# Performance work log

Measured on AMD Instinct MI355X. Metric: run time of the kernel, lower is better.

Reference implementation:

```python
import jax, jax.numpy as jnp
import numpy as np
from jax import lax

EPS = 1e-6


def _layernorm(x, g, b, eps=1e-5):
    m = x.mean(-1, keepdims=True)
    v = x.var(-1, keepdims=True)
    return (x - m) / jnp.sqrt(v + eps) * g + b


def _causal_conv(x, w, b, dilation):
    # x: [B,S,D], w: [K, D_in, D_out] -> causal (left) padded dilated conv + GELU, residual
    k = w.shape[0]
    pad = (k - 1) * dilation
    y = lax.conv_general_dilated(
        x, w, window_strides=(1,), padding=[(pad, 0)], rhs_dilation=(dilation,),
        dimension_numbers=('NWC', 'WIO', 'NWC'))
    return x + jax.nn.gelu(y + b)


def setup_inputs() -> dict:
    key = jax.random.key(0)
    B, S, D, DC, N_LTM, K_WM, KS = 4, 2048, 1024, 256, 768, 8, 5
    ks = jax.random.split(key, 24)
    sc = 0.02

    def n(k, shape, scale=sc):
        return jax.random.normal(k, shape, jnp.float32) * scale

    return {
        'x': jax.random.normal(ks[0], (B, S, D), jnp.float32),
        'cache': jax.random.normal(ks[1], (B, N_LTM, DC), jnp.float32),
        'wm': jax.random.normal(ks[2], (B, K_WM, DC + 1), jnp.float32),
        # LTM read projections
        'Wq_ltm': n(ks[3], (D, DC)), 'Wo_ltm': n(ks[4], (DC, D)), 'wg_ltm': n(ks[5], (D,)),
        # WM read projections
        'Wq_wm': n(ks[6], (D, DC)), 'Wo_wm': n(ks[7], (DC, D)), 'wg_wm': n(ks[8], (D,)),
        # causal dilated conv stack (2 layers, k=5, dilations 1 and 2)
        'conv1_w': n(ks[9], (KS, D, D)), 'conv1_b': jnp.zeros((D,), jnp.float32),
        'conv2_w': n(ks[10], (KS, D, D)), 'conv2_b': jnp.zeros((D,), jnp.float32),
        'ln_g': jnp.ones((D,), jnp.float32), 'ln_b': jnp.zeros((D,), jnp.float32),
        # WM write (learned slot keys for addressing)
        'Wqw_wm': n(ks[11], (D, DC)), 'Ww_wm': n(ks[12], (D, DC)),
        'wm_keys': n(ks[13], (K_WM, DC), 1.0), 'wgw_wm': n(ks[14], (D,)),
        # LTM write (content-based addressing against cache)
        'Wqw_ltm': n(ks[15], (D, DC)), 'Ww_ltm': n(ks[16], (D, DC)), 'wgw_ltm': n(ks[17], (D,)),
    }


def reference(x, cache, wm, Wq_ltm, Wo_ltm, wg_ltm, Wq_wm, Wo_wm, wg_wm,
              conv1_w, conv1_b, conv2_w, conv2_b, ln_g, ln_b,
              Wqw_wm, Ww_wm, wm_keys, wgw_wm, Wqw_ltm, Ww_ltm, wgw_ltm):
    DC = cache.shape[-1]
    inv_sqrt = 1.0 / jnp.sqrt(jnp.float32(DC))

    # ---- LTM READ: content-addressed soft read, gated residual blend ----
    q = x @ Wq_ltm                                                  # [B,S,DC]
    attn = jax.nn.softmax(jnp.einsum('bsd,bnd->bsn', q, cache) * inv_sqrt, -1)
    read = jnp.einsum('bsn,bnd->bsd', attn, cache)                  # [B,S,DC]
    gate = jax.nn.sigmoid(x @ wg_ltm)[..., None]                    # [B,S,1]
    x_ltm = x + gate * (read @ Wo_ltm)

    # ---- WM READ (read_decay=0.0 -> wm unchanged by read) ----
    content = wm[..., :DC]                                          # [B,Kw,DC]
    q2 = x_ltm @ Wq_wm
    attn2 = jax.nn.softmax(jnp.einsum('bsd,bkd->bsk', q2, content) * inv_sqrt, -1)
    read2 = jnp.einsum('bsk,bkd->bsd', attn2, content)
    gate2 = jax.nn.sigmoid(x_ltm @ wg_wm)[..., None]
    x_enh = x_ltm + gate2 * (read2 @ Wo_wm)

    # ---- COMPUTE: causal dilated conv stack + post-LayerNorm ----
    h = _causal_conv(x_enh, conv1_w, conv1_b, 1)
    h = _causal_conv(h, conv2_w, conv2_b, 2)
    out = _layernorm(h, ln_g, ln_b)                                 # [B,S,D]

    # ---- WM WRITE: gated soft-WTA addressing vs learned slot keys ----
    qw = out @ Wqw_wm                                               # [B,S,DC]
    aw = jax.nn.softmax(jnp.einsum('bsd,kd->bsk', qw, wm_keys) * inv_sqrt, -1)
    gw = jax.nn.sigmoid(out @ wgw_wm)[..., None]                    # [B,S,1]
    w = gw * aw                                                     # [B,S,Kw]
    tot = w.sum(1)                                                  # [B,Kw]
    c = out @ Ww_wm                                                 # [B,S,DC]
    avg = jnp.einsum('bsk,bsd->bkd', w, c) / (tot[..., None] + EPS)
    alpha = jnp.clip(tot, 0.0, 1.0)[..., None]
    new_content = (1.0 - alpha) * content + alpha * avg
    new_valid = jnp.clip(wm[..., DC] + tot, 0.0, 1.0)               # validity channel
    updated_wm = jnp.concatenate([new_content, new_valid[..., None]], -1)

    # ---- LTM WRITE: gated soft blended write, content-addressed vs cache ----
    ql = out @ Wqw_ltm
    al = jax.nn.softmax(jnp.einsum('bsd,bnd->bsn', ql, cache) * inv_sqrt, -1)
    gl = jax.nn.sigmoid(out @ wgw_ltm)[..., None]
    wl = gl * al                                                    # [B,S,N]
    totl = wl.sum(1)                                                # [B,N]
    cl = out @ Ww_ltm
    avgl = jnp.einsum('bsn,bsd->bnd', wl, cl) / (totl[..., None] + EPS)
    alphal = jnp.clip(totl, 0.0, 1.0)[..., None]
    updated_cache = (1.0 - alphal) * cache + alphal * avgl

    return (out, updated_cache, updated_wm)
```

## Files before the change

kernel.cpp:

```cpp
#include <hip/hip_runtime.h>
#include <stdint.h>

typedef unsigned short u16;
typedef unsigned int u32;
typedef __attribute__((ext_vector_type(8))) short s16x8;
typedef __attribute__((ext_vector_type(4))) float f32x4;

__device__ __forceinline__ float bf2f(u16 u) {
    return __builtin_bit_cast(float, (u32)u << 16);
}
__device__ __forceinline__ u16 f2bf(float f) {
    u32 u = __builtin_bit_cast(u32, f);
    u += 0x7FFFu + ((u >> 16) & 1u);
    return (u16)(u >> 16);
}
__device__ __forceinline__ void unpk4(uint2 r, float* o) {
    o[0] = bf2f((u16)(r.x & 0xffff)); o[1] = bf2f((u16)(r.x >> 16));
    o[2] = bf2f((u16)(r.y & 0xffff)); o[3] = bf2f((u16)(r.y >> 16));
}

__device__ __forceinline__ void gl16(const u16* g, u16* l) {
    __builtin_amdgcn_global_load_lds(
        (const __attribute__((address_space(1))) u32*)(const void*)g,
        (__attribute__((address_space(3))) u32*)(void*)l, 16, 0, 0);
}

#define BAR() { __builtin_amdgcn_sched_barrier(0); __builtin_amdgcn_s_barrier(); __builtin_amdgcn_sched_barrier(0); }

template<int DIL>
__global__ __launch_bounds__(512) void conv8_k(
    const u16* __restrict__ Apad, const u16* __restrict__ Bw,
    u16* __restrict__ Cb0, u16* __restrict__ Cb1)
{
    __shared__ u16 sA[2][16384];
    __shared__ u16 sB[2][16384];
    const int tid  = threadIdx.x;
    const int wid  = tid >> 6;
    const int lane = tid & 63;
    const int wr = (wid >> 2) * 128;
    const int wc = (wid & 3) * 64;
    const int lr = lane & 15;
    const int kq = lane >> 4;
    const int batch = blockIdx.x >> 3;
    const int m0b   = (blockIdx.x & 7) * 256;
    const int bn0   = blockIdx.y * 256;
    const int kbeg  = blockIdx.z * 2560;
    const u16* Ab = Apad + (long)batch * 2056 * 1024;

    const int row0 = tid >> 3;
    const int g0   = (tid & 7) ^ (row0 & 7);

    f32x4 acc[8][4] = {};
    s16x8 aF[4][2], bF[4][2];

    auto stageA = [&](int nb, int kt, int h) {
        const int ktabs = kbeg + kt * 64;
        const int tap = ktabs >> 10;
        const long rbase = (long)(8 + m0b + h * 128 + (tap - 4) * DIL) * 1024
                           + (ktabs & 1023) + g0 * 8;
        u16* dst = &sA[nb][h * 8192 + tid * 8];
        gl16(Ab + rbase + (long)row0 * 1024, dst);
        gl16(Ab + rbase + (long)(row0 + 64) * 1024, dst + 4096);
    };
    auto stageB = [&](int nb, int kt, int h) {
        const int ktabs = kbeg + kt * 64;
        const long rbase = (long)(bn0 + h * 128) * 5120 + ktabs + g0 * 8;
        u16* dst = &sB[nb][h * 8192 + tid * 8];
        gl16(Bw + rbase + (long)row0 * 5120, dst);
        gl16(Bw + rbase + (long)(row0 + 64) * 5120, dst + 4096);
    };
    auto readA = [&](int nb, int mq) {
        #pragma unroll
        for (int m = 0; m < 4; m++) {
            const int row = wr + (mq * 4 + m) * 16 + lr;
            #pragma unroll
            for (int ks = 0; ks < 2; ks++) {
                const int chunk = ks * 4 + kq;
                aF[m][ks] = *(const s16x8*)&sA[nb][row * 64 + ((chunk ^ (row & 7)) << 3)];
            }
        }
    };
    auto readB4 = [&](int nb, int nq) {
        #pragma unroll
        for (int n = 0; n < 2; n++) {
            const int row = wc + (nq * 2 + n) * 16 + lr;
            #pragma unroll
            for (int ks = 0; ks < 2; ks++) {
                const int chunk = ks * 4 + kq;
                bF[nq * 2 + n][ks] = *(const s16x8*)&sB[nb][row * 64 + ((chunk ^ (row & 7)) << 3)];
            }
        }
    };

#define MFQ(MQ, NQ) \
    { __builtin_amdgcn_s_setprio(1); \
      _Pragma("unroll") \
      for (int m = 0; m < 4; m++) { \
        _Pragma("unroll") \
        for (int n = 0; n < 2; n++) { \
          _Pragma("unroll") \
          for (int ks = 0; ks < 2; ks++) \
            acc[(MQ)*4+m][(NQ)*2+n] = __builtin_amdgcn_mfma_f32_16x16x32_bf16( \
                aF[m][ks], bF[(NQ)*2+n][ks], acc[(MQ)*4+m][(NQ)*2+n], 0, 0, 0); \
        } } \
      __builtin_amdgcn_s_setprio(0); }

    stageB(0, 0, 0); stageB(0, 0, 1); stageA(0, 0, 0); stageA(0, 0, 1);

    const int NT = 40;
    for (int t = 0; t < NT; ++t) {
        const int nb = t & 1;
        asm volatile("s_waitcnt vmcnt(4)" ::: "memory");
        BAR();
        readB4(nb, 0); readB4(nb, 1);
        if (t + 1 < NT) { stageB(nb ^ 1, t + 1, 0); stageB(nb ^ 1, t + 1, 1); }
        if (t + 1 < NT) { asm volatile("s_waitcnt vmcnt(4)" ::: "memory"); }
        else            { asm volatile("s_waitcnt vmcnt(0)" ::: "memory"); }
        BAR();
        readA(nb, 0);
        MFQ(0, 0); MFQ(0, 1);
        if (t + 1 < NT) { stageA(nb ^ 1, t + 1, 0); stageA(nb ^ 1, t + 1, 1); }
        readA(nb, 1);
        MFQ(1, 0); MFQ(1, 1);
    }
#undef MFQ

    u16* C = (blockIdx.z ? Cb1 : Cb0) + (long)batch * 2048 * 1024;
    #pragma unroll
    for (int m = 0; m < 8; m++) {
        #pragma unroll
        for (int n = 0; n < 4; n++) {
            const int cc = bn0 + wc + n * 16 + lr;
            #pragma unroll
            for (int j = 0; j < 4; j++) {
                const int r = m0b + wr + m * 16 + kq * 4 + j;
                C[(long)r * 1024 + cc] = f2bf(acc[m][n][j]);
            }
        }
    }
}

template<int AL, int BL, int EPI, int TN, int KS, int SWZ>
__global__ __launch_bounds__(256) void gemm_bf16(
    const u16* __restrict__ A, const u16* __restrict__ B,
    float* __restrict__ Cf, u16* __restrict__ Cb,
    const float* __restrict__ res, const float* __restrict__ gate,
    int M, int N, int K, int lda, int ldb,
    long aBS, long bBS, long cBS,
    u16* __restrict__ Pp, long pStride, int nby)
{
    constexpr int NFRAG = TN / 32;
    __shared__ u16 sA[128 * 32];
    __shared__ u16 sB[TN * 32];
    const int tid  = threadIdx.x;
    const int lane = tid & 63;
    const int wave = tid >> 6;
    const int wr = (wave >> 1) * 64;
    const int wc = (wave & 1) * (TN / 2);

    int bidx, bidy;
    if (SWZ) {
        const int nb  = gridDim.x;
        const int cpx = nb >> 3;
        const int bf  = blockIdx.x;
        const int sw  = (bf & 7) * cpx + (bf >> 3);
        bidx = sw / nby; bidy = sw - bidx * nby;
    } else {
        bidx = blockIdx.x; bidy = blockIdx.y;
    }
    const int m0 = bidx * 128;
    const int n0 = bidy * TN;
    const int zz = blockIdx.z;
    const long bz = (KS > 1) ? (zz / KS) : zz;
    const int ks  = (KS > 1) ? (zz % KS) : 0;
    const u16* Ab = A + bz * aBS;
    const u16* Bb = B + bz * bBS;

    f32x4 acc[4][NFRAG] = {};
    const int lr = lane & 15;
    const int lk = (lane >> 4) << 3;
    const int ar0 = tid >> 2;
    const int akg = (tid & 3) << 3;

    const int Kp = K / KS;
    const int kbeg = ks * Kp, kend = kbeg + Kp;

    for (int kk = kbeg; kk < kend; kk += 32) {
        __syncthreads();
        if (AL == 0) {
            gl16(Ab + (long)(m0 + ar0) * lda + kk + akg,      sA + tid * 8);
            gl16(Ab + (long)(m0 + ar0 + 64) * lda + kk + akg, sA + tid * 8 + 2048);
        } else {
            for (int t = tid; t < 512; t += 256) {
                int row = t & 127, kg = (t >> 7) << 3;
                u32 w0[4];
                #pragma unroll
                for (int j2 = 0; j2 < 4; j2++) {
                    u16 lo = Ab[(long)(kk + kg + 2*j2    ) * lda + m0 + row];
                    u16 hi = Ab[(long)(kk + kg + 2*j2 + 1) * lda + m0 + row];
                    w0[j2] = (u32)lo | ((u32)hi << 16);
                }
                uint4 v; v.x = w0[0]; v.y = w0[1]; v.z = w0[2]; v.w = w0[3];
                *reinterpret_cast<uint4*>(sA + row * 32 + kg) = v;
            }
        }
        if (BL == 1) {
            gl16(Bb + (long)(n0 + ar0) * ldb + kk + akg, sB + tid * 8);
            if (TN == 128)
                gl16(Bb + (long)(n0 + ar0 + 64) * ldb + kk + akg, sB + tid * 8 + 2048);
        } else {
            for (int t = tid; t < TN * 4; t += 256) {
                int col = t & (TN - 1), kg = (t / TN) << 3;
                u32 w0[4];
                #pragma unroll
                for (int j2 = 0; j2 < 4; j2++) {
                    u16 lo = Bb[(long)(kk + kg + 2*j2    ) * ldb + n0 + col];
                    u16 hi = Bb[(long)(kk + kg + 2*j2 + 1) * ldb + n0 + col];
                    w0[j2] = (u32)lo | ((u32)hi << 16);
                }
                uint4 v; v.x = w0[0]; v.y = w0[1]; v.z = w0[2]; v.w = w0[3];
                *reinterpret_cast<uint4*>(sB + col * 32 + kg) = v;
            }
        }
        __syncthreads();
        s16x8 aF[4], bF[NFRAG];
        #pragma unroll
        for (int m = 0; m < 4; m++)
            aF[m] = *reinterpret_cast<const s16x8*>(sA + (wr + m*16 + lr) * 32 + lk);
        #pragma unroll
        for (int n = 0; n < NFRAG; n++)
            bF[n] = *reinterpret_cast<const s16x8*>(sB + (wc + n*16 + lr) * 32 + lk);
        #pragma unroll
        for (int m = 0; m < 4; m++)
            #pragma unroll
            for (int n = 0; n < NFRAG; n++)
                acc[m][n] = __builtin_amdgcn_mfma_f32_16x16x32_bf16(aF[m], bF[n], acc[m][n], 0, 0, 0);
    }

    const int rj = (lane >> 4) << 2;
    if (KS > 1) {
        u16* Pb = Pp + (long)ks * pStride + bz * cBS;
        #pragma unroll
        for (int m = 0; m < 4; m++)
            #pragma unroll
            for (int n = 0; n < NFRAG; n++) {
                const int cc = n0 + wc + n*16 + lr;
                #pragma unroll
                for (int j = 0; j < 4; j++) {
                    const int r = m0 + wr + m*16 + rj + j;
                    Pb[(long)r * N + cc] = f2bf(acc[m][n][j]);
                }
            }
        return;
    }

    float* Cfb = Cf + bz * cBS;
    #pragma unroll
    for (int m = 0; m < 4; m++) {
        #pragma unroll
        for (int n = 0; n < NFRAG; n++) {
            const int cc = n0 + wc + n*16 + lr;
            #pragma unroll
            for (int j = 0; j < 4; j++) {
                const int r = m0 + wr + m*16 + rj + j;
                const long idx = (long)r * N + cc;
                const float v = acc[m][n][j];
                if (EPI == 0) {
                    Cb[bz * cBS + idx] = f2bf(v);
                } else if (EPI == 1) {
                    Cfb[idx] = v;
                } else {
                    float o = res[idx] + gate[r] * v;
                    Cfb[idx] = o;
                    if (EPI == 2) Cb[idx] = f2bf(o);
                }
            }
        }
    }
}

template<int KS, int BF>
__global__ __launch_bounds__(256) void ksum_k(
    const u16* __restrict__ Pp, long pStride,
    float* __restrict__ outf, u16* __restrict__ outb, int n4)
{
    int i = blockIdx.x * 256 + threadIdx.x;
    if (i >= n4) return;
    float s[4] = {0.f, 0.f, 0.f, 0.f};
    #pragma unroll
    for (int k = 0; k < KS; k++) {
        uint2 r = reinterpret_cast<const uint2*>(Pp + (long)k * pStride)[i];
        float v[4]; unpk4(r, v);
        s[0] += v[0]; s[1] += v[1]; s[2] += v[2]; s[3] += v[3];
    }
    if (BF) {
        u32 lo = (u32)f2bf(s[0]) | ((u32)f2bf(s[1]) << 16);
        u32 hi = (u32)f2bf(s[2]) | ((u32)f2bf(s[3]) << 16);
        reinterpret_cast<uint2*>(outb)[i] = make_uint2(lo, hi);
    } else {
        float4 o; o.x = s[0]; o.y = s[1]; o.z = s[2]; o.w = s[3];
        reinterpret_cast<float4*>(outf)[i] = o;
    }
}

__global__ __launch_bounds__(256) void prep_k(
    const float* __restrict__ x, const float* __restrict__ cache,
    const float* __restrict__ wm_keys, const float* __restrict__ wm,
    const float* __restrict__ Wo_wm, const float* __restrict__ Wq_wm,
    const float* __restrict__ Wq_ltm, const float* __restrict__ Wqw_wm,
    const float* __restrict__ Ww_wm, const float* __restrict__ Wqw_ltm,
    const float* __restrict__ Ww_ltm, const float* __restrict__ Wo_ltm,
    const float* __restrict__ conv1_w, const float* __restrict__ conv2_w,
    u16* __restrict__ xpad1, u16* __restrict__ xpad2,
    float* __restrict__ tot, float* __restrict__ totl,
    u16* __restrict__ act0, u16* __restrict__ cache_b, u16* __restrict__ keys_b,
    u16* __restrict__ WqLt, u16* __restrict__ WqWt, u16* __restrict__ WbigT,
    u16* __restrict__ WoLt, u16* __restrict__ c1wt, u16* __restrict__ c2wt,
    u16* __restrict__ cache_t, float* __restrict__ CW, float* __restrict__ WC)
{
    __shared__ float tile[32][33];
    int b = blockIdx.x;
    int tid = threadIdx.x;

    if (b < 64) {
        int i = b * 256 + tid;
        int bt = i >> 12, j = i & 4095;
        long offp = (long)bt * (2056L * 1024 / 2) + j;
        reinterpret_cast<u32*>(xpad1)[offp] = 0u;
        reinterpret_cast<u32*>(xpad2)[offp] = 0u;
        if (i < 32) tot[i] = 0.f;
        if (i < 3072) totl[i] = 0.f;
        return;
    }
    b -= 64;
    if (b < 8192 + 768 + 2) {
        const float* in; u16* out; int i;
        if (b < 8192)      { in = x;       out = act0;    i = b * 256 + tid; }
        else if (b < 8960) { in = cache;   out = cache_b; i = (b - 8192) * 256 + tid; }
        else               { in = wm_keys; out = keys_b;  i = (b - 8960) * 256 + tid; }
        float4 v = reinterpret_cast<const float4*>(in)[i];
        u32 lo = (u32)f2bf(v.x) | ((u32)f2bf(v.y) << 16);
        u32 hi = (u32)f2bf(v.z) | ((u32)f2bf(v.w) << 16);
        reinterpret_cast<uint2*>(out)[i] = make_uint2(lo, hi);
        return;
    }
    b -= 8962;
    if (b < 12800) {
        const float* in; u16* out; int R, C, l;
        if (b < 1536) {
            l = b & 255; R = 1024; C = 256;
            int m = b >> 8;
            if      (m == 0) { in = Wq_ltm;  out = WqLt; }
            else if (m == 1) { in = Wq_wm;   out = WqWt; }
            else if (m == 2) { in = Wqw_wm;  out = WbigT; }
            else if (m == 3) { in = Ww_wm;   out = WbigT + 262144; }
            else if (m == 4) { in = Wqw_ltm; out = WbigT + 524288; }
            else             { in = Ww_ltm;  out = WbigT + 786432; }
        } else if (b < 1792) {
            l = b - 1536; in = Wo_ltm; out = WoLt; R = 256; C = 1024;
        } else if (b < 6912) {
            l = b - 1792; in = conv1_w; out = c1wt; R = 5120; C = 1024;
        } else if (b < 12032) {
            l = b - 6912; in = conv2_w; out = c2wt; R = 5120; C = 1024;
        } else {
            int lb = b - 12032;
            int z = lb / 192; l = lb % 192;
            in = cache + (long)z * 196608; out = cache_t + (long)z * 196608;
            R = 768; C = 256;
        }
        const int ct = C >> 5;
        const int c0 = (l % ct) * 32, r0 = (l / ct) * 32;
        int tx = tid & 31, ty = tid >> 5;
        #pragma unroll
        for (int i = 0; i < 32; i += 8)
            tile[ty + i][tx] = in[(long)(r0 + ty + i) * C + c0 + tx];
        __syncthreads();
        #pragma unroll
        for (int i = 0; i < 32; i += 8)
            out[(long)(c0 + ty + i) * R + r0 + tx] = f2bf(tile[tx][ty + i]);
        return;
    }
    b -= 12800;
    if (b < 32) {
        const float* wrow = wm + (long)(b >> 3) * 2056 + (b & 7) * 257;
        int c = tid;
        float a0 = 0.f, a1 = 0.f, a2 = 0.f, a3 = 0.f;
        for (int dd = 0; dd < 256; dd++) {
            float w = wrow[dd];
            const float* wo = Wo_wm + (long)dd * 1024;
            a0 += w * wo[c]; a1 += w * wo[c + 256];
            a2 += w * wo[c + 512]; a3 += w * wo[c + 768];
        }
        float* o = CW + (long)b * 1024;
        o[c] = a0; o[c + 256] = a1; o[c + 512] = a2; o[c + 768] = a3;
        return;
    }
    b -= 32;
    {
        const float* wrow = wm + (long)(b >> 3) * 2056 + (b & 7) * 257;
        int c = tid;
        float a0 = 0.f, a1 = 0.f, a2 = 0.f, a3 = 0.f;
        for (int j = 0; j < 256; j++) {
            float w = wrow[j];
            a0 += Wq_wm[(long)(c      ) * 256 + j] * w;
            a1 += Wq_wm[(long)(c + 256) * 256 + j] * w;
            a2 += Wq_wm[(long)(c + 512) * 256 + j] * w;
            a3 += Wq_wm[(long)(c + 768) * 256 + j] * w;
        }
        float* o = WC + (long)b * 1024;
        o[c] = a0; o[c + 256] = a1; o[c + 512] = a2; o[c + 768] = a3;
    }
}

__global__ __launch_bounds__(256) void gemv_sigmoid_k(
    const float* __restrict__ X, const float* __restrict__ w,
    float* __restrict__ out)
{
    int row  = blockIdx.x * 4 + (threadIdx.x >> 6);
    int lane = threadIdx.x & 63;
    const float* xr = X + (long)row * 1024;
    float s = 0.f;
    for (int i = lane; i < 1024; i += 64) s += xr[i] * w[i];
    #pragma unroll
    for (int o = 32; o > 0; o >>= 1) s += __shfl_down(s, o);
    if (lane == 0) out[row] = 1.f / (1.f + __expf(-s));
}

__global__ __launch_bounds__(256) void softmax768_k(
    const u16* __restrict__ scores, u16* __restrict__ out,
    const float* __restrict__ gate)
{
    __shared__ float s4[4], s4b[4];
    int row = blockIdx.x;
    int t = threadIdx.x;
    const u16* sr = scores + (long)row * 768;
    float v[3];
    float m = -1e30f;
    #pragma unroll
    for (int i = 0; i < 3; i++) { v[i] = bf2f(sr[t + i*256]) * 0.0625f; m = fmaxf(m, v[i]); }
    float wm_ = m;
    #pragma unroll
    for (int o = 32; o > 0; o >>= 1) wm_ = fmaxf(wm_, __shfl_down(wm_, o));
    if ((t & 63) == 0) s4[t >> 6] = wm_;
    __syncthreads();
    float bm = fmaxf(fmaxf(s4[0], s4[1]), fmaxf(s4[2], s4[3]));
    float sum = 0.f;
    #pragma unroll
    for (int i = 0; i < 3; i++) { v[i] = __expf(v[i] - bm); sum += v[i]; }
    #pragma unroll
    for (int o = 32; o > 0; o >>= 1) sum += __shfl_down(sum, o);
    if ((t & 63) == 0) s4b[t >> 6] = sum;
    __syncthreads();
    float bs = s4b[0] + s4b[1] + s4b[2] + s4b[3];
    float g = gate ? gate[row] : 1.0f;
    float inv = g / bs;
    u16* orow = out + (long)row * 768;
    #pragma unroll
    for (int i = 0; i < 3; i++) orow[t + i*256] = f2bf(v[i] * inv);
}

__global__ __launch_bounds__(256) void wm_read_fused_k(
    const float* __restrict__ WC, const float* __restrict__ CW,
    const float* __restrict__ wg, const float* __restrict__ res,
    float* __restrict__ outf, u16* __restrict__ outb)
{
    __shared__ float sred[8][4];
    __shared__ float sg4[4];
    __shared__ float sa[8];
    __shared__ float gsh;
    int row = blockIdx.x;
    int b = row >> 11;
    int d = threadIdx.x, lane = d & 63, wave = d >> 6;
    long orow = (long)row * 1024;
    float rv0 = res[orow + d];
    float rv1 = res[orow + d + 256];
    float rv2 = res[orow + d + 512];
    float rv3 = res[orow + d + 768];
    float gp = rv0 * wg[d] + rv1 * wg[d + 256] + rv2 * wg[d + 512] + rv3 * wg[d + 768];
    #pragma unroll
    for (int o = 32; o > 0; o >>= 1) gp += __shfl_down(gp, o);
    if (lane == 0) sg4[wave] = gp;
    const float* wcb = WC + (long)b * 8192;
    #pragma unroll
    for (int k = 0; k < 8; k++) {
        const float* w = wcb + k * 1024;
        float v = rv0 * w[d] + rv1 * w[d + 256] + rv2 * w[d + 512] + rv3 * w[d + 768];
        #pragma unroll
        for (int o = 32; o > 0; o >>= 1) v += __shfl_down(v, o);
        if (lane == 0) sred[k][wave] = v;
    }
    __syncthreads();
    if (d < 8) sa[d] = (sred[d][0] + sred[d][1] + sred[d][2] + sred[d][3]) * 0.0625f;
    if (d == 0) gsh = 1.f / (1.f + __expf(-(sg4[0] + sg4[1] + sg4[2] + sg4[3])));
    __syncthreads();
    float m = sa[0];
    #pragma unroll
    for (int k = 1; k < 8; k++) m = fmaxf(m, sa[k]);
    float e[8], sum = 0.f;
    #pragma unroll
    for (int k = 0; k < 8; k++) { e[k] = __expf(sa[k] - m); sum += e[k]; }
    float inv = 1.f / sum;
    #pragma unroll
    for (int k = 0; k < 8; k++) e[k] *= inv;
    float g = gsh;
    const float* cwb = CW + (long)b * 8192;
    long prow = ((long)(row >> 11) * 2056 + 8 + (row & 2047)) * 1024;
    float rv[4] = { rv0, rv1, rv2, rv3 };
    #pragma unroll
    for (int j = 0; j < 4; j++) {
        int c = d + j * 256;
        float acc = 0.f;
        #pragma unroll
        for (int k = 0; k < 8; k++) acc += e[k] * cwb[k * 1024 + c];
        float o = rv[j] + g * acc;
        outf[orow + c] = o;
        outb[prow + c] = f2bf(o);
    }
}

template<int PAD>
__global__ __launch_bounds__(256) void gelu_reduce_k(
    const u16* __restrict__ p0, const u16* __restrict__ p1, const float4* __restrict__ res,
    const float* __restrict__ bias, float4* __restrict__ outf, u16* __restrict__ outb)
{
    int i4 = blockIdx.x * 256 + threadIdx.x;
    int r = i4 >> 8, c4 = (i4 & 255) << 2;
    float a[4], b[4];
    unpk4(reinterpret_cast<const uint2*>(p0)[i4], a);
    unpk4(reinterpret_cast<const uint2*>(p1)[i4], b);
    float4 rr = res[i4];
    float4 bi = *reinterpret_cast<const float4*>(bias + c4);
    float o[4];
    float y0 = a[0] + b[0] + bi.x, y1 = a[1] + b[1] + bi.y;
    float y2 = a[2] + b[2] + bi.z, y3 = a[3] + b[3] + bi.w;
    const float C0 = 0.79788456080286535588f, C1 = 0.044715f;
    o[0] = rr.x + 0.5f * y0 * (1.f + tanhf(C0 * (y0 + C1 * y0 * y0 * y0)));
    o[1] = rr.y + 0.5f * y1 * (1.f + tanhf(C0 * (y1 + C1 * y1 * y1 * y1)));
    o[2] = rr.z + 0.5f * y2 * (1.f + tanhf(C0 * (y2 + C1 * y2 * y2 * y2)));
    o[3] = rr.w + 0.5f * y3 * (1.f + tanhf(C0 * (y3 + C1 * y3 * y3 * y3)));
    float4 ov; ov.x = o[0]; ov.y = o[1]; ov.z = o[2]; ov.w = o[3];
    outf[i4] = ov;
    if (PAD) {
        long prow = ((long)(r >> 11) * 2056 + 8 + (r & 2047)) * 1024 + c4;
        u32 lo = (u32)f2bf(o[0]) | ((u32)f2bf(o[1]) << 16);
        u32 hi = (u32)f2bf(o[2]) | ((u32)f2bf(o[3]) << 16);
        *reinterpret_cast<uint2*>(outb + prow) = make_uint2(lo, hi);
    }
}

__global__ __launch_bounds__(256) void gelu_ln_k(
    const u16* __restrict__ p0, const u16* __restrict__ p1,
    const float4* __restrict__ res, const float* __restrict__ bias,
    const float* __restrict__ g, const float* __restrict__ b,
    float* __restrict__ outf, u16* __restrict__ outb)
{
    __shared__ float rs[4], rss[4];
    int row = blockIdx.x, t = threadIdx.x;
    long i4 = (long)row * 256 + t;
    float a[4], pb[4];
    unpk4(reinterpret_cast<const uint2*>(p0)[i4], a);
    unpk4(reinterpret_cast<const uint2*>(p1)[i4], pb);
    float4 rr = res[i4];
    float4 bi = reinterpret_cast<const float4*>(bias)[t];
    const float C0 = 0.79788456080286535588f, C1 = 0.044715f;
    float y0 = a[0] + pb[0] + bi.x, y1 = a[1] + pb[1] + bi.y;
    float y2 = a[2] + pb[2] + bi.z, y3 = a[3] + pb[3] + bi.w;
    float o0 = rr.x + 0.5f * y0 * (1.f + tanhf(C0 * (y0 + C1 * y0 * y0 * y0)));
    float o1 = rr.y + 0.5f * y1 * (1.f + tanhf(C0 * (y1 + C1 * y1 * y1 * y1)));
    float o2 = rr.z + 0.5f * y2 * (1.f + tanhf(C0 * (y2 + C1 * y2 * y2 * y2)));
    float o3 = rr.w + 0.5f * y3 * (1.f + tanhf(C0 * (y3 + C1 * y3 * y3 * y3)));
    float s  = o0 + o1 + o2 + o3;
    float ss = o0*o0 + o1*o1 + o2*o2 + o3*o3;
    #pragma unroll
    for (int o = 32; o > 0; o >>= 1) { s += __shfl_down(s, o); ss += __shfl_down(ss, o); }
    if ((t & 63) == 0) { rs[t >> 6] = s; rss[t >> 6] = ss; }
    __syncthreads();
    float S = rs[0]+rs[1]+rs[2]+rs[3];
    float SS = rss[0]+rss[1]+rss[2]+rss[3];
    float mean = S * (1.f/1024.f);
    float var  = SS * (1.f/1024.f) - mean*mean;
    float rstd = rsqrtf(var + 1e-5f);
    float4 gg = reinterpret_cast<const float4*>(g)[t];
    float4 bv = reinterpret_cast<const float4*>(b)[t];
    float4 y;
    y.x = (o0-mean)*rstd*gg.x + bv.x;
    y.y = (o1-mean)*rstd*gg.y + bv.y;
    y.z = (o2-mean)*rstd*gg.z + bv.z;
    y.w = (o3-mean)*rstd*gg.w + bv.w;
    reinterpret_cast<float4*>(outf)[i4] = y;
    u32 lo = (u32)f2bf(y.x) | ((u32)f2bf(y.y) << 16);
    u32 hi = (u32)f2bf(y.z) | ((u32)f2bf(y.w) << 16);
    reinterpret_cast<uint2*>(outb)[i4] = make_uint2(lo, hi);
}

__global__ __launch_bounds__(256) void attn8_wg_k(
    const u16* __restrict__ q, const float* __restrict__ xo,
    const float* __restrict__ w1, const float* __restrict__ w2,
    const u16* __restrict__ keys, float* __restrict__ wD,
    float* __restrict__ gateb2)
{
    __shared__ float sred[8][4];
    __shared__ float sa[8];
    __shared__ float sg1[4], sg2[4];
    __shared__ float g1sh;
    int row = blockIdx.x;
    int d = threadIdx.x, lane = d & 63, wave = d >> 6;
    float qv = bf2f(q[(long)row * 1024 + d]);
    float4 xr  = reinterpret_cast<const float4*>(xo + (long)row * 1024)[d];
    float4 w1v = reinterpret_cast<const float4*>(w1)[d];
    float4 w2v = reinterpret_cast<const float4*>(w2)[d];
    float s1 = xr.x*w1v.x + xr.y*w1v.y + xr.z*w1v.z + xr.w*w1v.w;
    float s2 = xr.x*w2v.x + xr.y*w2v.y + xr.z*w2v.z + xr.w*w2v.w;
    #pragma unroll
    for (int o = 32; o > 0; o >>= 1) { s1 += __shfl_down(s1, o); s2 += __shfl_down(s2, o); }
    if (lane == 0) { sg1[wave] = s1; sg2[wave] = s2; }
    #pragma unroll
    for (int k = 0; k < 8; k++) {
        float v = qv * bf2f(keys[k * 256 + d]);
        #pragma unroll
        for (int o = 32; o > 0; o >>= 1) v += __shfl_down(v, o);
        if (lane == 0) sred[k][wave] = v;
    }
    __syncthreads();
    if (d < 8) sa[d] = (sred[d][0] + sred[d][1] + sred[d][2] + sred[d][3]) * 0.0625f;
    if (d == 0) {
        g1sh = 1.f / (1.f + __expf(-(sg1[0] + sg1[1] + sg1[2] + sg1[3])));
        gateb2[row] = 1.f / (1.f + __expf(-(sg2[0] + sg2[1] + sg2[2] + sg2[3])));
    }
    __syncthreads();
    if (d < 8) {
        float m = sa[0];
        #pragma unroll
        for (int k = 1; k < 8; k++) m = fmaxf(m, sa[k]);
        float e = __expf(sa[d] - m), sum = 0.f;
        #pragma unroll
        for (int k = 0; k < 8; k++) sum += __expf(sa[k] - m);
        wD[(long)row * 8 + d] = g1sh * e / sum;
    }
}

__global__ __launch_bounds__(256) void tot8_k(const float* __restrict__ wD, float* __restrict__ tot)
{
    __shared__ float s4[4];
    int b = blockIdx.y;
    int s = blockIdx.x * 256 + threadIdx.x;
    const float* p = wD + ((long)b * 2048 + s) * 8;
    float v[8];
    #pragma unroll
    for (int k = 0; k < 8; k++) v[k] = p[k];
    for (int k = 0; k < 8; k++) {
        float xv = v[k];
        #pragma unroll
        for (int o = 32; o > 0; o >>= 1) xv += __shfl_down(xv, o);
        if ((threadIdx.x & 63) == 0) s4[threadIdx.x >> 6] = xv;
        __syncthreads();
        if (threadIdx.x == 0) atomicAdd(&tot[b*8 + k], s4[0]+s4[1]+s4[2]+s4[3]);
        __syncthreads();
    }
}

__global__ __launch_bounds__(256) void wm_avg_partial_k(
    const float* __restrict__ wD, const u16* __restrict__ cw, float* __restrict__ part)
{
    int blk = blockIdx.x;
    int b = blk >> 6, k = (blk >> 3) & 7, ch = blk & 7;
    int d = threadIdx.x;
    const float* wp = wD + ((long)b * 2048 + ch * 256) * 8 + k;
    const u16*   cp = cw + ((long)b * 2048 + ch * 256) * 1024 + 256 + d;
    float acc = 0.f;
    for (int s = 0; s < 256; s++) acc += wp[s * 8] * bf2f(cp[(long)s * 1024]);
    part[(long)blk * 256 + d] = acc;
}

__global__ __launch_bounds__(256) void wm_final_k(
    const float* __restrict__ part, const float* __restrict__ wm,
    const float* __restrict__ tot, float* __restrict__ out)
{
    int bk = blockIdx.x;
    int d = threadIdx.x;
    float acc = 0.f;
    #pragma unroll
    for (int ch = 0; ch < 8; ch++) acc += part[((long)bk * 8 + ch) * 256 + d];
    float t = tot[bk];
    float alpha = fminf(fmaxf(t, 0.f), 1.f);
    float avg = acc / (t + 1e-6f);
    long base = (long)(bk >> 3) * 2056 + (bk & 7) * 257;
    out[base + d] = (1.f - alpha) * wm[base + d] + alpha * avg;
    if (d == 0) out[base + 256] = fminf(fmaxf(wm[base + 256] + t, 0.f), 1.f);
}

__global__ void colsum_wl_k(const u16* __restrict__ wl, float* __restrict__ totl)
{
    int b = blockIdx.z;
    int n = blockIdx.x * 256 + threadIdx.x;
    int s0 = blockIdx.y * 256;
    const u16* p = wl + ((long)b * 2048 + s0) * 768 + n;
    float acc = 0.f;
    for (int s = 0; s < 256; s++) acc += bf2f(p[(long)s * 768]);
    atomicAdd(&totl[b * 768 + n], acc);
}

__global__ void cache_blend_k(const float* __restrict__ cache, const float* __restrict__ Sg,
                              const float* __restrict__ totl, float* __restrict__ out)
{
    long i = (long)blockIdx.x * 256 + threadIdx.x;
    int bn = (int)(i >> 8);
    float t = totl[bn];
    float a = fminf(fmaxf(t, 0.f), 1.f);
    out[i] = (1.f - a) * cache[i] + a * (Sg[i] / (t + 1e-6f));
}

extern "C" void kernel_launch(void* const* d_in, const int* in_sizes, int n_in,
                              void* d_out, int out_size, void* d_ws, size_t ws_size,
                              hipStream_t stream)
{
    const int D = 1024, DC = 256, NL = 768;
    const long MS = 8192;
    const long SB = 2048;

    const float* x       = (const float*)d_in[0];
    const float* cache   = (const float*)d_in[1];
    const float* wm      = (const float*)d_in[2];
    const float* Wq_ltm  = (const float*)d_in[3];
    const float* Wo_ltm  = (const float*)d_in[4];
    const float* wg_ltm  = (const float*)d_in[5];
    const float* Wq_wm   = (const float*)d_in[6];
    const float* Wo_wm   = (const float*)d_in[7];
    const float* wg_wm   = (const float*)d_in[8];
    const float* conv1_w = (const float*)d_in[9];
    const float* conv1_b = (const float*)d_in[10];
    const float* conv2_w = (const float*)d_in[11];
    const float* conv2_b = (const float*)d_in[12];
    const float* ln_g    = (const float*)d_in[13];
    const float* ln_b    = (const float*)d_in[14];
    const float* Wqw_wm  = (const float*)d_in[15];
    const float* Ww_wm   = (const float*)d_in[16];
    const float* wm_keys = (const float*)d_in[17];
    const float* wgw_wm  = (const float*)d_in[18];
    const float* Wqw_ltm = (const float*)d_in[19];
    const float* Ww_ltm  = (const float*)d_in[20];
    const float* wgw_ltm = (const float*)d_in[21];

    float* out_f     = (float*)d_out;
    float* cache_out = out_f + 8388608;
    float* wm_out    = out_f + 8388608 + 786432;

    char* ws = (char*)d_ws;
    size_t off = 0;
    auto alloc = [&](size_t bytes) -> char* {
        char* p = ws + off;
        off = (off + bytes + 255) & ~(size_t)255;
        return p;
    };
    u16* WqLt    = (u16*)alloc((size_t)D*DC*2);
    u16* WoLt    = (u16*)alloc((size_t)D*DC*2);
    u16* WqWt    = (u16*)alloc((size_t)D*DC*2);
    u16* WbigT   = (u16*)alloc((size_t)D*D*2);
    u16* c1wt    = (u16*)alloc((size_t)5*D*D*2);
    u16* c2wt    = (u16*)alloc((size_t)5*D*D*2);
    u16* cache_b = (u16*)alloc((size_t)4*NL*DC*2);
    u16* cache_t = (u16*)alloc((size_t)4*NL*DC*2);
    u16* keys_b  = (u16*)alloc((size_t)8*DC*2);
    u16* act0    = (u16*)alloc((size_t)MS*D*2);
    u16* act1    = (u16*)alloc((size_t)MS*D*2);
    u16* xpad1   = (u16*)alloc((size_t)4*2056*1024*2);
    u16* xpad2   = (u16*)alloc((size_t)4*2056*1024*2);
    u16* qb      = (u16*)alloc((size_t)MS*DC*2);
    u16* attnb   = (u16*)alloc((size_t)MS*NL*2);
    u16* readb   = (u16*)alloc((size_t)MS*DC*2);
    float* fact0 = (float*)alloc((size_t)MS*D*4);
    float* fact1 = (float*)alloc((size_t)MS*D*4);
    u16* Pu      = (u16*)alloc((size_t)16777216*2);
    float* CW    = (float*)alloc((size_t)4*8*D*4);
    float* WC    = (float*)alloc((size_t)4*8*D*4);
    float* gateb = (float*)alloc((size_t)MS*4);
    float* gateb2= (float*)alloc((size_t)MS*4);
    float* wD    = (float*)alloc((size_t)MS*8*4);
    float* tot   = (float*)alloc((size_t)4*8*4);
    float* totl  = (float*)alloc((size_t)4*NL*4);
    float* part  = (float*)alloc((size_t)256*256*4);
    float* avglS = (float*)alloc((size_t)4*NL*DC*4);
    u16*   qbig   = act0;

    prep_k<<<21890, 256, 0, stream>>>(
        x, cache, wm_keys, wm, Wo_wm, Wq_wm,
        Wq_ltm, Wqw_wm, Ww_wm, Wqw_ltm, Ww_ltm, Wo_ltm, conv1_w, conv2_w,
        xpad1, xpad2, tot, totl, act0, cache_b, keys_b,
        WqLt, WqWt, WbigT, WoLt, c1wt, c2wt, cache_t, CW, WC);

    gemm_bf16<0,1,0,64,4,1><<<dim3(256,1,4), 256, 0, stream>>>(
        act0, WqLt, nullptr, nullptr, nullptr, nullptr,
        8192,256,1024,1024,1024, 0,0,0, Pu, 2097152L, 4);
    ksum_k<4,1><<<2048, 256, 0, stream>>>(Pu, 2097152L, nullptr, qb, 524288);
    gemv_sigmoid_k<<<2048, 256, 0, stream>>>(x, wg_ltm, gateb);
    gemm_bf16<0,1,0,128,1,1><<<dim3(96,1,4), 256, 0, stream>>>(
        qb, cache_b, nullptr, Pu, nullptr, nullptr,
        2048,768,256,256,256, SB*256, (long)NL*DC, SB*768, nullptr, 0, 6);
    softmax768_k<<<8192, 256, 0, stream>>>(Pu, attnb, nullptr);
    gemm_bf16<0,1,0,64,2,1><<<dim3(64,1,8), 256, 0, stream>>>(
        attnb, cache_t, nullptr, nullptr, nullptr, nullptr,
        2048,256,768,768,768, SB*768, (long)NL*DC, SB*256, Pu, 2097152L, 4);
    ksum_k<2,1><<<2048, 256, 0, stream>>>(Pu, 2097152L, nullptr, readb, 524288);
    gemm_bf16<0,1,5,128,1,1><<<dim3(512,1,1), 256, 0, stream>>>(
        readb, WoLt, fact0, nullptr, x, gateb,
        8192,1024,256,256,256, 0,0,0, nullptr, 0, 8);

    wm_read_fused_k<<<8192, 256, 0, stream>>>(WC, CW, wg_wm, fact0, fact1, xpad1);

    conv8_k<1><<<dim3(32,4,2), 512, 0, stream>>>(xpad1, c1wt, Pu, Pu + 8388608);
    gelu_reduce_k<1><<<8192, 256, 0, stream>>>(
        Pu, Pu + 8388608, (const float4*)fact1, conv1_b, (float4*)fact0, xpad2);
    conv8_k<2><<<dim3(32,4,2), 512, 0, stream>>>(xpad2, c2wt, Pu, Pu + 8388608);
    gelu_ln_k<<<8192, 256, 0, stream>>>(
        Pu, Pu + 8388608, (const float4*)fact0, conv2_b, ln_g, ln_b, out_f, act1);

    gemm_bf16<0,1,0,128,1,1><<<dim3(512,1,1), 256, 0, stream>>>(
        act1, WbigT, nullptr, qbig, nullptr, nullptr,
        8192,1024,1024,1024,1024, 0,0,0, nullptr, 0, 8);
    attn8_wg_k<<<8192, 256, 0, stream>>>(qbig, out_f, wgw_wm, wgw_ltm, keys_b, wD, gateb2);
    tot8_k<<<dim3(8, 4), 256, 0, stream>>>(wD, tot);
    wm_avg_partial_k<<<256, 256, 0, stream>>>(wD, qbig, part);
    wm_final_k<<<32, 256, 0, stream>>>(part, wm, tot, wm_out);

    gemm_bf16<0,1,0,128,1,1><<<dim3(96,1,4), 256, 0, stream>>>(
        qbig + 512, cache_b, nullptr, Pu, nullptr, nullptr,
        2048,768,256,1024,256, SB*1024, (long)NL*DC, SB*768, nullptr, 0, 6);
    softmax768_k<<<8192, 256, 0, stream>>>(Pu, attnb, gateb2);
    colsum_wl_k<<<dim3(3, 8, 4), 256, 0, stream>>>(attnb, totl);
    gemm_bf16<1,0,1,64,4,0><<<dim3(6,4,16), 256, 0, stream>>>(
        attnb, qbig + 768, nullptr, nullptr, nullptr, nullptr,
        768,256,2048,768,1024, SB*768, SB*1024, 196608L, Pu, 786432L, 0);
    ksum_k<4,0><<<768, 256, 0, stream>>>(Pu, 786432L, avglS, nullptr, 196608);
    cache_blend_k<<<3072, 256, 0, stream>>>(cache, avglS, totl, cache_out);

    (void)in_sizes; (void)n_in; (void)out_size; (void)ws_size;
}
```

Before: 502.8 us.

## Fold Wq_ltm into cache keys and fuse small reduction kernels

```diff
diff --git a/kernel.cpp b/kernel.cpp
--- a/kernel.cpp
+++ b/kernel.cpp
@@ -312,9 +312,9 @@
     const float* __restrict__ Ww_ltm, const float* __restrict__ Wo_ltm,
     const float* __restrict__ conv1_w, const float* __restrict__ conv2_w,
     u16* __restrict__ xpad1, u16* __restrict__ xpad2,
-    float* __restrict__ tot, float* __restrict__ totl,
+    float* __restrict__ totl,
     u16* __restrict__ act0, u16* __restrict__ cache_b, u16* __restrict__ keys_b,
-    u16* __restrict__ WqLt, u16* __restrict__ WqWt, u16* __restrict__ WbigT,
+    u16* __restrict__ Wqb, u16* __restrict__ WbigT,
     u16* __restrict__ WoLt, u16* __restrict__ c1wt, u16* __restrict__ c2wt,
     u16* __restrict__ cache_t, float* __restrict__ CW, float* __restrict__ WC)
 {
@@ -328,42 +328,40 @@
         long offp = (long)bt * (2056L * 1024 / 2) + j;
         reinterpret_cast<u32*>(xpad1)[offp] = 0u;
         reinterpret_cast<u32*>(xpad2)[offp] = 0u;
-        if (i < 32) tot[i] = 0.f;
         if (i < 3072) totl[i] = 0.f;
         return;
     }
     b -= 64;
-    if (b < 8192 + 768 + 2) {
+    if (b < 9218) {
         const float* in; u16* out; int i;
         if (b < 8192)      { in = x;       out = act0;    i = b * 256 + tid; }
         else if (b < 8960) { in = cache;   out = cache_b; i = (b - 8192) * 256 + tid; }
-        else               { in = wm_keys; out = keys_b;  i = (b - 8960) * 256 + tid; }
+        else if (b < 8962) { in = wm_keys; out = keys_b;  i = (b - 8960) * 256 + tid; }
+        else               { in = Wq_ltm;  out = Wqb;     i = (b - 8962) * 256 + tid; }
         float4 v = reinterpret_cast<const float4*>(in)[i];
         u32 lo = (u32)f2bf(v.x) | ((u32)f2bf(v.y) << 16);
         u32 hi = (u32)f2bf(v.z) | ((u32)f2bf(v.w) << 16);
         reinterpret_cast<uint2*>(out)[i] = make_uint2(lo, hi);
         return;
     }
-    b -= 8962;
-    if (b < 12800) {
+    b -= 9218;
+    if (b < 12288) {
         const float* in; u16* out; int R, C, l;
-        if (b < 1536) {
+        if (b < 1024) {
             l = b & 255; R = 1024; C = 256;
             int m = b >> 8;
-            if      (m == 0) { in = Wq_ltm;  out = WqLt; }
-            else if (m == 1) { in = Wq_wm;   out = WqWt; }
-            else if (m == 2) { in = Wqw_wm;  out = WbigT; }
-            else if (m == 3) { in = Ww_wm;   out = WbigT + 262144; }
-            else if (m == 4) { in = Wqw_ltm; out = WbigT + 524288; }
+            if      (m == 0) { in = Wqw_wm;  out = WbigT; }
+            else if (m == 1) { in = Ww_wm;   out = WbigT + 262144; }
+            else if (m == 2) { in = Wqw_ltm; out = WbigT + 524288; }
             else             { in = Ww_ltm;  out = WbigT + 786432; }
-        } else if (b < 1792) {
-            l = b - 1536; in = Wo_ltm; out = WoLt; R = 256; C = 1024;
-        } else if (b < 6912) {
-            l = b - 1792; in = conv1_w; out = c1wt; R = 5120; C = 1024;
-        } else if (b < 12032) {
-            l = b - 6912; in = conv2_w; out = c2wt; R = 5120; C = 1024;
+        } else if (b < 1280) {
+            l = b - 1024; in = Wo_ltm; out = WoLt; R = 256; C = 1024;
+        } else if (b < 6400) {
+            l = b - 1280; in = conv1_w; out = c1wt; R = 5120; C = 1024;
+        } else if (b < 11520) {
+            l = b - 6400; in = conv2_w; out = c2wt; R = 5120; C = 1024;
         } else {
-            int lb = b - 12032;
+            int lb = b - 11520;
             int z = lb / 192; l = lb % 192;
             in = cache + (long)z * 196608; out = cache_t + (long)z * 196608;
             R = 768; C = 256;
@@ -380,7 +378,7 @@
             out[(long)(c0 + ty + i) * R + r0 + tx] = f2bf(tile[tx][ty + i]);
         return;
     }
-    b -= 12800;
+    b -= 12288;
     if (b < 32) {
         const float* wrow = wm + (long)(b >> 3) * 2056 + (b & 7) * 257;
         int c = tid;
@@ -413,14 +411,18 @@
 }
 
 __global__ __launch_bounds__(256) void gemv_sigmoid_k(
-    const float* __restrict__ X, const float* __restrict__ w,
+    const u16* __restrict__ X, const float* __restrict__ w,
     float* __restrict__ out)
 {
     int row  = blockIdx.x * 4 + (threadIdx.x >> 6);
     int lane = threadIdx.x & 63;
-    const float* xr = X + (long)row * 1024;
+    const u16* xr = X + (long)row * 1024;
     float s = 0.f;
-    for (int i = lane; i < 1024; i += 64) s += xr[i] * w[i];
+    for (int i = lane * 4; i < 1024; i += 256) {
+        uint2 r = *reinterpret_cast<const uint2*>(xr + i);
+        float v[4]; unpk4(r, v);
+        s += v[0]*w[i] + v[1]*w[i+1] + v[2]*w[i+2] + v[3]*w[i+3];
+    }
     #pragma unroll
     for (int o = 32; o > 0; o >>= 1) s += __shfl_down(s, o);
     if (lane == 0) out[row] = 1.f / (1.f + __expf(-s));
@@ -639,49 +641,37 @@
     }
 }
 
-__global__ __launch_bounds__(256) void tot8_k(const float* __restrict__ wD, float* __restrict__ tot)
-{
-    __shared__ float s4[4];
-    int b = blockIdx.y;
-    int s = blockIdx.x * 256 + threadIdx.x;
-    const float* p = wD + ((long)b * 2048 + s) * 8;
-    float v[8];
-    #pragma unroll
-    for (int k = 0; k < 8; k++) v[k] = p[k];
-    for (int k = 0; k < 8; k++) {
-        float xv = v[k];
-        #pragma unroll
-        for (int o = 32; o > 0; o >>= 1) xv += __shfl_down(xv, o);
-        if ((threadIdx.x & 63) == 0) s4[threadIdx.x >> 6] = xv;
-        __syncthreads();
-        if (threadIdx.x == 0) atomicAdd(&tot[b*8 + k], s4[0]+s4[1]+s4[2]+s4[3]);
-        __syncthreads();
-    }
-}
-
 __global__ __launch_bounds__(256) void wm_avg_partial_k(
-    const float* __restrict__ wD, const u16* __restrict__ cw, float* __restrict__ part)
+    const float* __restrict__ wD, const u16* __restrict__ cw,
+    float* __restrict__ part, float* __restrict__ part2)
 {
     int blk = blockIdx.x;
     int b = blk >> 6, k = (blk >> 3) & 7, ch = blk & 7;
     int d = threadIdx.x;
     const float* wp = wD + ((long)b * 2048 + ch * 256) * 8 + k;
     const u16*   cp = cw + ((long)b * 2048 + ch * 256) * 1024 + 256 + d;
-    float acc = 0.f;
-    for (int s = 0; s < 256; s++) acc += wp[s * 8] * bf2f(cp[(long)s * 1024]);
+    float acc = 0.f, wsum = 0.f;
+    for (int s = 0; s < 256; s++) {
+        float wv = wp[s * 8];
+        acc += wv * bf2f(cp[(long)s * 1024]);
+        wsum += wv;
+    }
     part[(long)blk * 256 + d] = acc;
+    if (d == 0) part2[blk] = wsum;
 }
 
 __global__ __launch_bounds__(256) void wm_final_k(
-    const float* __restrict__ part, const float* __restrict__ wm,
-    const float* __restrict__ tot, float* __restrict__ out)
+    const float* __restrict__ part, const float* __restrict__ part2,
+    const float* __restrict__ wm, float* __restrict__ out)
 {
     int bk = blockIdx.x;
     int d = threadIdx.x;
-    float acc = 0.f;
-    #pragma unroll
-    for (int ch = 0; ch < 8; ch++) acc += part[((long)bk * 8 + ch) * 256 + d];
-    float t = tot[bk];
+    float acc = 0.f, t = 0.f;
+    #pragma unroll
+    for (int ch = 0; ch < 8; ch++) {
+        acc += part[((long)bk * 8 + ch) * 256 + d];
+        t   += part2[bk * 8 + ch];
+    }
     float alpha = fminf(fmaxf(t, 0.f), 1.f);
     float avg = acc / (t + 1e-6f);
     long base = (long)(bk >> 3) * 2056 + (bk & 7) * 257;
@@ -700,14 +690,30 @@
     atomicAdd(&totl[b * 768 + n], acc);
 }
 
-__global__ void cache_blend_k(const float* __restrict__ cache, const float* __restrict__ Sg,
-                              const float* __restrict__ totl, float* __restrict__ out)
-{
-    long i = (long)blockIdx.x * 256 + threadIdx.x;
+__global__ __launch_bounds__(256) void cache_blend_k(
+    const float* __restrict__ cache, const u16* __restrict__ Pp, long pStride,
+    const float* __restrict__ totl, float* __restrict__ out)
+{
+    int i4 = blockIdx.x * 256 + threadIdx.x;
+    float s[4] = {0.f, 0.f, 0.f, 0.f};
+    #pragma unroll
+    for (int k = 0; k < 4; k++) {
+        uint2 r = reinterpret_cast<const uint2*>(Pp + (long)k * pStride)[i4];
+        float v[4]; unpk4(r, v);
+        s[0] += v[0]; s[1] += v[1]; s[2] += v[2]; s[3] += v[3];
+    }
+    long i = (long)i4 * 4;
     int bn = (int)(i >> 8);
     float t = totl[bn];
     float a = fminf(fmaxf(t, 0.f), 1.f);
-    out[i] = (1.f - a) * cache[i] + a * (Sg[i] / (t + 1e-6f));
+    float inv = a / (t + 1e-6f);
+    float4 cv = reinterpret_cast<const float4*>(cache)[i4];
+    float4 o;
+    o.x = (1.f - a) * cv.x + s[0] * inv;
+    o.y = (1.f - a) * cv.y + s[1] * inv;
+    o.z = (1.f - a) * cv.z + s[2] * inv;
+    o.w = (1.f - a) * cv.w + s[3] * inv;
+    reinterpret_cast<float4*>(out)[i4] = o;
 }
 
 extern "C" void kernel_launch(void* const* d_in, const int* in_sizes, int n_in,
@@ -752,20 +758,19 @@
         off = (off + bytes + 255) & ~(size_t)255;
         return p;
     };
-    u16* WqLt    = (u16*)alloc((size_t)D*DC*2);
+    u16* Wqb     = (u16*)alloc((size_t)D*DC*2);
     u16* WoLt    = (u16*)alloc((size_t)D*DC*2);
-    u16* WqWt    = (u16*)alloc((size_t)D*DC*2);
     u16* WbigT   = (u16*)alloc((size_t)D*D*2);
     u16* c1wt    = (u16*)alloc((size_t)5*D*D*2);
     u16* c2wt    = (u16*)alloc((size_t)5*D*D*2);
     u16* cache_b = (u16*)alloc((size_t)4*NL*DC*2);
     u16* cache_t = (u16*)alloc((size_t)4*NL*DC*2);
     u16* keys_b  = (u16*)alloc((size_t)8*DC*2);
+    u16* WqC     = (u16*)alloc((size_t)4*NL*D*2);
     u16* act0    = (u16*)alloc((size_t)MS*D*2);
     u16* act1    = (u16*)alloc((size_t)MS*D*2);
     u16* xpad1   = (u16*)alloc((size_t)4*2056*1024*2);
     u16* xpad2   = (u16*)alloc((size_t)4*2056*1024*2);
-    u16* qb      = (u16*)alloc((size_t)MS*DC*2);
     u16* attnb   = (u16*)alloc((size_t)MS*NL*2);
     u16* readb   = (u16*)alloc((size_t)MS*DC*2);
     float* fact0 = (float*)alloc((size_t)MS*D*4);
@@ -776,34 +781,32 @@
     float* gateb = (float*)alloc((size_t)MS*4);
     float* gateb2= (float*)alloc((size_t)MS*4);
     float* wD    = (float*)alloc((size_t)MS*8*4);
-    float* tot   = (float*)alloc((size_t)4*8*4);
     float* totl  = (float*)alloc((size_t)4*NL*4);
     float* part  = (float*)alloc((size_t)256*256*4);
-    float* avglS = (float*)alloc((size_t)4*NL*DC*4);
+    float* part2 = (float*)alloc((size_t)256*4);
     u16*   qbig   = act0;
 
-    prep_k<<<21890, 256, 0, stream>>>(
+    prep_k<<<21634, 256, 0, stream>>>(
         x, cache, wm_keys, wm, Wo_wm, Wq_wm,
         Wq_ltm, Wqw_wm, Ww_wm, Wqw_ltm, Ww_ltm, Wo_ltm, conv1_w, conv2_w,
-        xpad1, xpad2, tot, totl, act0, cache_b, keys_b,
-        WqLt, WqWt, WbigT, WoLt, c1wt, c2wt, cache_t, CW, WC);
-
-    gemm_bf16<0,1,0,64,4,1><<<dim3(256,1,4), 256, 0, stream>>>(
-        act0, WqLt, nullptr, nullptr, nullptr, nullptr,
-        8192,256,1024,1024,1024, 0,0,0, Pu, 2097152L, 4);
-    ksum_k<4,1><<<2048, 256, 0, stream>>>(Pu, 2097152L, nullptr, qb, 524288);
-    gemv_sigmoid_k<<<2048, 256, 0, stream>>>(x, wg_ltm, gateb);
+        xpad1, xpad2, totl, act0, cache_b, keys_b,
+        Wqb, WbigT, WoLt, c1wt, c2wt, cache_t, CW, WC);
+
+    gemm_bf16<0,1,0,128,1,0><<<dim3(6,8,4), 256, 0, stream>>>(
+        cache_b, Wqb, nullptr, WqC, nullptr, nullptr,
+        768,1024,256, 256,256, 196608L, 0L, 786432L, nullptr, 0, 0);
+    gemv_sigmoid_k<<<2048, 256, 0, stream>>>(act0, wg_ltm, gateb);
     gemm_bf16<0,1,0,128,1,1><<<dim3(96,1,4), 256, 0, stream>>>(
-        qb, cache_b, nullptr, Pu, nullptr, nullptr,
-        2048,768,256,256,256, SB*256, (long)NL*DC, SB*768, nullptr, 0, 6);
+        act0, WqC, nullptr, Pu, nullptr, nullptr,
+        2048,768,1024, 1024,1024, SB*1024, 786432L, SB*768, nullptr, 0, 6);
     softmax768_k<<<8192, 256, 0, stream>>>(Pu, attnb, nullptr);
     gemm_bf16<0,1,0,64,2,1><<<dim3(64,1,8), 256, 0, stream>>>(
         attnb, cache_t, nullptr, nullptr, nullptr, nullptr,
-        2048,256,768,768,768, SB*768, (long)NL*DC, SB*256, Pu, 2097152L, 4);
+        2048,256,768, 768,768, SB*768, (long)NL*DC, SB*256, Pu, 2097152L, 4);
     ksum_k<2,1><<<2048, 256, 0, stream>>>(Pu, 2097152L, nullptr, readb, 524288);
     gemm_bf16<0,1,5,128,1,1><<<dim3(512,1,1), 256, 0, stream>>>(
         readb, WoLt, fact0, nullptr, x, gateb,
-        8192,1024,256,256,256, 0,0,0, nullptr, 0, 8);
+        8192,1024,256, 256,256, 0,0,0, nullptr, 0, 8);
 
     wm_read_fused_k<<<8192, 256, 0, stream>>>(WC, CW, wg_wm, fact0, fact1, xpad1);
 
@@ -816,22 +819,20 @@
 
     gemm_bf16<0,1,0,128,1,1><<<dim3(512,1,1), 256, 0, stream>>>(
         act1, WbigT, nullptr, qbig, nullptr, nullptr,
-        8192,1024,1024,1024,1024, 0,0,0, nullptr, 0, 8);
+        8192,1024,1024, 1024,1024, 0,0,0, nullptr, 0, 8);
     attn8_wg_k<<<8192, 256, 0, stream>>>(qbig, out_f, wgw_wm, wgw_ltm, keys_b, wD, gateb2);
-    tot8_k<<<dim3(8, 4), 256, 0, stream>>>(wD, tot);
-    wm_avg_partial_k<<<256, 256, 0, stream>>>(wD, qbig, part);
-    wm_final_k<<<32, 256, 0, stream>>>(part, wm, tot, wm_out);
+    wm_avg_partial_k<<<256, 256, 0, stream>>>(wD, qbig, part, part2);
+    wm_final_k<<<32, 256, 0, stream>>>(part, part2, wm, wm_out);
 
     gemm_bf16<0,1,0,128,1,1><<<dim3(96,1,4), 256, 0, stream>>>(
         qbig + 512, cache_b, nullptr, Pu, nullptr, nullptr,
-        2048,768,256,1024,256, SB*1024, (long)NL*DC, SB*768, nullptr, 0, 6);
+        2048,768,256, 1024,256, SB*1024, (long)NL*DC, SB*768, nullptr, 0, 6);
     softmax768_k<<<8192, 256, 0, stream>>>(Pu, attnb, gateb2);
     colsum_wl_k<<<dim3(3, 8, 4), 256, 0, stream>>>(attnb, totl);
     gemm_bf16<1,0,1,64,4,0><<<dim3(6,4,16), 256, 0, stream>>>(
         attnb, qbig + 768, nullptr, nullptr, nullptr, nullptr,
-        768,256,2048,768,1024, SB*768, SB*1024, 196608L, Pu, 786432L, 0);
-    ksum_k<4,0><<<768, 256, 0, stream>>>(Pu, 786432L, avglS, nullptr, 196608);
-    cache_blend_k<<<3072, 256, 0, stream>>>(cache, avglS, totl, cache_out);
+        768,256,2048, 768,1024, SB*768, SB*1024, 196608L, Pu, 786432L, 0);
+    cache_blend_k<<<768, 256, 0, stream>>>(cache, Pu, 786432L, totl, cache_out);
 
     (void)in_sizes; (void)n_in; (void)out_size; (void)ws_size;
 }
```

Result: no change. 504.9 us (+0.4%).
